# Kernel tuning notes

Hardware: AMD Instinct MI355X
Metric: run time of the kernel (lower is better)

The kernel has to match this reference:

```python
import jax, jax.numpy as jnp
import numpy as np

B, T, C, H = 4, 2048, 1024, 16
D = C // H  # head_size = 64


def _layernorm(x, g, b, eps=1e-5):
    mu = jnp.mean(x, axis=-1, keepdims=True)
    var = jnp.var(x, axis=-1, keepdims=True)
    return (x - mu) * jax.lax.rsqrt(var + eps) * g + b


def setup_inputs() -> dict:
    key = jax.random.key(0)
    ks = jax.random.split(key, 12)
    s = 0.02
    return {
        "x": jax.random.normal(ks[0], (B, T, C), dtype=jnp.float32),
        "Wq": jax.random.normal(ks[1], (C, C), dtype=jnp.float32) * s,
        "Wk": jax.random.normal(ks[2], (C, C), dtype=jnp.float32) * s,
        "Wv": jax.random.normal(ks[3], (C, C), dtype=jnp.float32) * s,
        "Wo": jax.random.normal(ks[4], (C, C), dtype=jnp.float32) * s,
        "bo": jnp.zeros((C,), dtype=jnp.float32),
        "ln1_g": jnp.ones((C,), dtype=jnp.float32),
        "ln1_b": jnp.zeros((C,), dtype=jnp.float32),
        "ln2_g": jnp.ones((C,), dtype=jnp.float32),
        "ln2_b": jnp.zeros((C,), dtype=jnp.float32),
        "W1": jax.random.normal(ks[5], (C, 4 * C), dtype=jnp.float32) * s,
        "b1": jnp.zeros((4 * C,), dtype=jnp.float32),
        "W2": jax.random.normal(ks[6], (4 * C, C), dtype=jnp.float32) * s,
        "b2": jnp.zeros((C,), dtype=jnp.float32),
    }


def reference(x, Wq, Wk, Wv, Wo, bo, ln1_g, ln1_b, ln2_g, ln2_b, W1, b1, W2, b2):
    # --- self-attention branch (pre-LN) ---
    h = _layernorm(x, ln1_g, ln1_b)
    q = (h @ Wq).reshape(B, T, H, D)
    k = (h @ Wk).reshape(B, T, H, D)
    v = (h @ Wv).reshape(B, T, H, D)
    scores = jnp.einsum("bqhd,bkhd->bhqk", q, k) * (D ** -0.5)
    causal = jnp.tril(jnp.ones((T, T), dtype=bool))
    scores = jnp.where(causal, scores, -jnp.inf)
    attn = jax.nn.softmax(scores, axis=-1)  # dropout=0 in eval
    out = jnp.einsum("bhqk,bkhd->bqhd", attn, v).reshape(B, T, C)
    x = x + (out @ Wo + bo)
    # --- feed-forward branch (pre-LN) ---
    h2 = _layernorm(x, ln2_g, ln2_b)
    ff = jax.nn.relu(h2 @ W1 + b1) @ W2 + b2
    return x + ff
```

## Files before the change

### kernel.cpp

```cpp
#include <hip/hip_runtime.h>
#include <hip/hip_bf16.h>
#include <math.h>

#define Bsz 4
#define Tsz 2048
#define Csz 1024
#define Hsz 16
#define Dsz 64
#define Msz (Bsz * Tsz)

typedef __attribute__((ext_vector_type(8))) __bf16 bf16x8;
typedef __attribute__((ext_vector_type(2))) __bf16 bf16x2;
typedef __attribute__((ext_vector_type(4))) float f32x4;

#define GLOBAL_AS __attribute__((address_space(1)))
#define LDS_AS    __attribute__((address_space(3)))


__device__ __forceinline__ float block_sum256(float v, float* sh) {
#pragma unroll
    for (int o = 32; o > 0; o >>= 1) v += __shfl_down(v, o, 64);
    int lane = threadIdx.x & 63, w = threadIdx.x >> 6;
    __syncthreads();
    if (lane == 0) sh[w] = v;
    __syncthreads();
    return sh[0] + sh[1] + sh[2] + sh[3];
}


__global__ __launch_bounds__(256) void layernorm_bf16(const float* __restrict__ x,
                                                      const float* __restrict__ g,
                                                      const float* __restrict__ b,
                                                      __bf16* __restrict__ out) {
    __shared__ float sh[4];
    const int row = blockIdx.x;
    const float* xr = x + (size_t)row * Csz;
    float v[4];
    float s = 0.f, ss = 0.f;
#pragma unroll
    for (int i = 0; i < 4; i++) {
        v[i] = xr[threadIdx.x + i * 256];
        s += v[i];
        ss += v[i] * v[i];
    }
    float tot = block_sum256(s, sh);
    float mean = tot * (1.0f / Csz);
    float tot2 = block_sum256(ss, sh);
    float var = tot2 * (1.0f / Csz) - mean * mean;
    float inv = rsqrtf(var + 1e-5f);
    __bf16* orow = out + (size_t)row * Csz;
#pragma unroll
    for (int i = 0; i < 4; i++) {
        int c = threadIdx.x + i * 256;
        orow[c] = (__bf16)((v[i] - mean) * inv * g[c] + b[c]);
    }
}


__global__ __launch_bounds__(256) void transpose_bf16(const float* __restrict__ W,
                                                      __bf16* __restrict__ Wt,
                                                      int K, int N) {
    __shared__ float t[32][33];
    const int k0 = blockIdx.y * 32, n0 = blockIdx.x * 32;
    const int c = threadIdx.x & 31, r8 = threadIdx.x >> 5;
#pragma unroll
    for (int it = 0; it < 4; it++) {
        int r = r8 + it * 8;
        t[r][c] = W[(size_t)(k0 + r) * N + n0 + c];
    }
    __syncthreads();
#pragma unroll
    for (int it = 0; it < 4; it++) {
        int r = r8 + it * 8;
        Wt[(size_t)(n0 + r) * K + k0 + c] = (__bf16)t[c][r];
    }
}


__global__ __launch_bounds__(256) void gemm_bf16(const __bf16* __restrict__ A,
                                                 const __bf16* __restrict__ Bt,
                                                 float* __restrict__ Cf,
                                                 __bf16* __restrict__ Cb,
                                                 int M, int N, int K,
                                                 const float* __restrict__ bias,
                                                 const float* __restrict__ resid,
                                                 int do_relu) {
    __shared__ __bf16 As[128 * 32];
    __shared__ __bf16 Bs[128 * 32];

    const int tid = threadIdx.x;
    const int lane = tid & 63;
    const int w = tid >> 6;
    const int rowBase = blockIdx.y * 128;
    const int colBase = blockIdx.x * 128;
    const int wr = (w & 1) * 64;
    const int wc = (w >> 1) * 64;

    const int m16 = lane & 15;
    const int kg = lane >> 4;

    f32x4 acc[4][4] = {};

    const int ldRow = lane >> 2;
    const int ldCol = (lane & 3) * 8;

    for (int k0 = 0; k0 < K; k0 += 32) {
        __syncthreads();
#pragma unroll
        for (int j = 0; j < 2; j++) {
            int rA = w * 32 + j * 16 + ldRow;
            const __bf16* ga = A + (size_t)(rowBase + rA) * K + k0 + ldCol;
            __builtin_amdgcn_global_load_lds((const GLOBAL_AS unsigned int*)ga,
                                             (LDS_AS unsigned int*)(As + rA * 32),
                                             16, 0, 0);
            int rB = w * 32 + j * 16 + ldRow;
            const __bf16* gb = Bt + (size_t)(colBase + rB) * K + k0 + ldCol;
            __builtin_amdgcn_global_load_lds((const GLOBAL_AS unsigned int*)gb,
                                             (LDS_AS unsigned int*)(Bs + rB * 32),
                                             16, 0, 0);
        }
        __syncthreads();

        bf16x8 af[4], bfv[4];
#pragma unroll
        for (int i = 0; i < 4; i++)
            af[i] = *(const bf16x8*)(As + (wr + i * 16 + m16) * 32 + kg * 8);
#pragma unroll
        for (int j = 0; j < 4; j++)
            bfv[j] = *(const bf16x8*)(Bs + (wc + j * 16 + m16) * 32 + kg * 8);
#pragma unroll
        for (int i = 0; i < 4; i++)
#pragma unroll
            for (int j = 0; j < 4; j++)
                acc[i][j] = __builtin_amdgcn_mfma_f32_16x16x32_bf16(af[i], bfv[j], acc[i][j], 0, 0, 0);
    }

    const int cn = lane & 15;
    const int rq = (lane >> 4) * 4;
    float bj[4];
#pragma unroll
    for (int j = 0; j < 4; j++)
        bj[j] = bias ? bias[colBase + wc + j * 16 + cn] : 0.f;

#pragma unroll
    for (int i = 0; i < 4; i++) {
#pragma unroll
        for (int r = 0; r < 4; r++) {
            int m = rowBase + wr + i * 16 + rq + r;
            size_t rowOff = (size_t)m * N;
#pragma unroll
            for (int j = 0; j < 4; j++) {
                int n = colBase + wc + j * 16 + cn;
                float v = acc[i][j][r] + bj[j];
                if (do_relu) v = fmaxf(v, 0.f);
                if (resid) v += resid[rowOff + n];
                if (Cf) Cf[rowOff + n] = v;
                if (Cb) Cb[rowOff + n] = (__bf16)v;
            }
        }
    }
}


__global__ __launch_bounds__(256, 4) void attn_mfma(const __bf16* __restrict__ QKV,
                                                    __bf16* __restrict__ O) {
    __shared__ __bf16 Ks[64 * 64];
    __shared__ __bf16 Vt[64 * 72];
    __shared__ __bf16 Ps[128 * 72];

    const int tid = threadIdx.x;
    const int lane = tid & 63;
    const int w = tid >> 6;
    const int bh = blockIdx.x;
    const int b = bh >> 4, h = bh & 15;
    const int qt = (int)gridDim.y - 1 - (int)blockIdx.y;
    const int qbase = qt * 128;
    const int ld3C = 3 * Csz;

    const __bf16* Qg = QKV + (size_t)(b * Tsz) * ld3C + h * Dsz;
    const __bf16* Kg = Qg + Csz;
    const __bf16* Vg = Qg + 2 * Csz;

    const int m16 = lane & 15;
    const int kg = lane >> 4;
    const int rq = kg * 4;
    const int wrow = w * 32;
    const int swz = m16 & 7;

    bf16x8 aq[2][2];
#pragma unroll
    for (int i = 0; i < 2; i++)
#pragma unroll
        for (int s = 0; s < 2; s++)
            aq[i][s] = *(const bf16x8*)(Qg + (size_t)(qbase + wrow + i * 16 + m16) * ld3C + (s * 4 + kg) * 8);

    const int sr = lane >> 3;
    const int sc = lane & 7;
    const int gcs = sc ^ sr;

    const int kp = (lane & 31) * 2;
    const int dg = w * 2 + (lane >> 5);

    f32x4 Oacc[2][4];
    float l_part[2][4];
#pragma unroll
    for (int i = 0; i < 2; i++)
#pragma unroll
        for (int j = 0; j < 4; j++) Oacc[i][j] = (f32x4){0.f, 0.f, 0.f, 0.f};
#pragma unroll
    for (int i = 0; i < 2; i++)
#pragma unroll
        for (int r = 0; r < 4; r++) l_part[i][r] = 0.f;

    const float CEXP = 0.18033688f;

    const int nkt = 2 * qt + 2;
    for (int kt = 0; kt < nkt; kt++) {
        const int kbase = kt * 64;
        __syncthreads();

#pragma unroll
        for (int it = 0; it < 2; it++) {
            int lr = w * 16 + it * 8 + sr;
            const __bf16* src = Kg + (size_t)(kbase + lr) * ld3C + gcs * 8;
            __builtin_amdgcn_global_load_lds((const GLOBAL_AS unsigned int*)src,
                                             (LDS_AS unsigned int*)(Ks + (w * 16 + it * 8) * 64),
                                             16, 0, 0);
        }
        bf16x8 v0 = *(const bf16x8*)(Vg + (size_t)(kbase + kp) * ld3C + dg * 8);
        bf16x8 v1 = *(const bf16x8*)(Vg + (size_t)(kbase + kp + 1) * ld3C + dg * 8);
        __syncthreads();

        f32x4 S[2][4];
#pragma unroll
        for (int i = 0; i < 2; i++)
#pragma unroll
            for (int j = 0; j < 4; j++) S[i][j] = (f32x4){0.f, 0.f, 0.f, 0.f};
#pragma unroll
        for (int s = 0; s < 2; s++) {
            bf16x8 bk[4];
#pragma unroll
            for (int j = 0; j < 4; j++)
                bk[j] = *(const bf16x8*)(Ks + (j * 16 + m16) * 64 + (((s * 4 + kg) ^ swz) * 8));
#pragma unroll
            for (int i = 0; i < 2; i++)
#pragma unroll
                for (int j = 0; j < 4; j++)
                    S[i][j] = __builtin_amdgcn_mfma_f32_16x16x32_bf16(aq[i][s], bk[j], S[i][j], 0, 0, 0);
        }

        const bool domask = (kt >= 2 * qt);
#pragma unroll
        for (int i = 0; i < 2; i++) {
#pragma unroll
            for (int j = 0; j < 4; j++) {
#pragma unroll
                for (int r = 0; r < 4; r++) {
                    float arg = S[i][j][r] * CEXP;
                    if (domask && (kbase + j * 16 + m16 > qbase + wrow + i * 16 + rq + r))
                        arg = -INFINITY;
                    float e = exp2f(arg);
                    S[i][j][r] = e;
                    l_part[i][r] += e;
                }
            }
        }

#pragma unroll
        for (int i = 0; i < 2; i++)
#pragma unroll
            for (int j = 0; j < 4; j++)
#pragma unroll
                for (int r = 0; r < 4; r++)
                    Ps[(wrow + i * 16 + rq + r) * 72 + j * 16 + m16] = (__bf16)S[i][j][r];
#pragma unroll
        for (int e = 0; e < 8; e++) {
            bf16x2 pr;
            pr[0] = v0[e];
            pr[1] = v1[e];
            *(bf16x2*)(Vt + (dg * 8 + e) * 72 + kp) = pr;
        }
        __syncthreads();

#pragma unroll
        for (int s = 0; s < 2; s++) {
            bf16x8 ap[2], bv[4];
#pragma unroll
            for (int i = 0; i < 2; i++)
                ap[i] = *(const bf16x8*)(Ps + (wrow + i * 16 + m16) * 72 + s * 32 + kg * 8);
#pragma unroll
            for (int j = 0; j < 4; j++)
                bv[j] = *(const bf16x8*)(Vt + (j * 16 + m16) * 72 + s * 32 + kg * 8);
#pragma unroll
            for (int i = 0; i < 2; i++)
#pragma unroll
                for (int j = 0; j < 4; j++)
                    Oacc[i][j] = __builtin_amdgcn_mfma_f32_16x16x32_bf16(ap[i], bv[j], Oacc[i][j], 0, 0, 0);
        }
    }

#pragma unroll
    for (int i = 0; i < 2; i++) {
#pragma unroll
        for (int r = 0; r < 4; r++) {
            float l = l_part[i][r];
#pragma unroll
            for (int msk = 1; msk < 16; msk <<= 1) l += __shfl_xor(l, msk, 64);
            const float inv = 1.0f / l;
            const int qrow = qbase + wrow + i * 16 + rq + r;
            __bf16* orow = O + (size_t)(b * Tsz + qrow) * Csz + h * Dsz;
#pragma unroll
            for (int j = 0; j < 4; j++)
                orow[j * 16 + m16] = (__bf16)(Oacc[i][j][r] * inv);
        }
    }
}


extern "C" void kernel_launch(void* const* d_in, const int* in_sizes, int n_in,
                              void* d_out, int out_size, void* d_ws, size_t ws_size,
                              hipStream_t stream) {
    const float* x     = (const float*)d_in[0];
    const float* Wq    = (const float*)d_in[1];
    const float* Wk    = (const float*)d_in[2];
    const float* Wv    = (const float*)d_in[3];
    const float* Wo    = (const float*)d_in[4];
    const float* bo    = (const float*)d_in[5];
    const float* ln1_g = (const float*)d_in[6];
    const float* ln1_b = (const float*)d_in[7];
    const float* ln2_g = (const float*)d_in[8];
    const float* ln2_b = (const float*)d_in[9];
    const float* W1    = (const float*)d_in[10];
    const float* b1    = (const float*)d_in[11];
    const float* W2    = (const float*)d_in[12];
    const float* b2    = (const float*)d_in[13];
    float* out = (float*)d_out;

    const size_t MB = 1u << 20;
    char* w = (char*)d_ws;
    __bf16* h    = (__bf16*)(w + 0);
    __bf16* Wqkv = (__bf16*)(w + 16 * MB);
    __bf16* Wot  = (__bf16*)(w + 22 * MB);
    __bf16* W1t  = (__bf16*)(w + 24 * MB);
    __bf16* W2t  = (__bf16*)(w + 32 * MB);
    __bf16* QKVb = (__bf16*)(w + 40 * MB);
    __bf16* ff1  = (__bf16*)(w + 40 * MB);
    __bf16* AO   = (__bf16*)(w + 104 * MB);

    transpose_bf16<<<dim3(Csz / 32, Csz / 32), 256, 0, stream>>>(Wq, Wqkv, Csz, Csz);
    transpose_bf16<<<dim3(Csz / 32, Csz / 32), 256, 0, stream>>>(Wk, Wqkv + 1024 * 1024, Csz, Csz);
    transpose_bf16<<<dim3(Csz / 32, Csz / 32), 256, 0, stream>>>(Wv, Wqkv + 2048 * 1024, Csz, Csz);
    transpose_bf16<<<dim3(Csz / 32, Csz / 32), 256, 0, stream>>>(Wo, Wot, Csz, Csz);
    transpose_bf16<<<dim3(4 * Csz / 32, Csz / 32), 256, 0, stream>>>(W1, W1t, Csz, 4 * Csz);
    transpose_bf16<<<dim3(Csz / 32, 4 * Csz / 32), 256, 0, stream>>>(W2, W2t, 4 * Csz, Csz);

    layernorm_bf16<<<Msz, 256, 0, stream>>>(x, ln1_g, ln1_b, h);
    gemm_bf16<<<dim3(3 * Csz / 128, Msz / 128), 256, 0, stream>>>(h, Wqkv, nullptr, QKVb, Msz, 3 * Csz, Csz, nullptr, nullptr, 0);
    attn_mfma<<<dim3(Bsz * Hsz, Tsz / 128), 256, 0, stream>>>(QKVb, AO);
    gemm_bf16<<<dim3(Csz / 128, Msz / 128), 256, 0, stream>>>(AO, Wot, out, nullptr, Msz, Csz, Csz, bo, x, 0);

    layernorm_bf16<<<Msz, 256, 0, stream>>>(out, ln2_g, ln2_b, h);
    gemm_bf16<<<dim3(4 * Csz / 128, Msz / 128), 256, 0, stream>>>(h, W1t, nullptr, ff1, Msz, 4 * Csz, Csz, b1, nullptr, 1);
    gemm_bf16<<<dim3(Csz / 128, Msz / 128), 256, 0, stream>>>(ff1, W2t, out, nullptr, Msz, Csz, 4 * Csz, b2, out, 0);
}
```

Baseline: 599.4 us.

## Use swizzled BK=64 GEMM tiles, split-K FFN down-proj, batch weight transposes

GEMM K-tile doubles to 64 with an XOR-swizzled LDS layout to halve barrier count per K and reduce bank conflicts. The FFN second GEMM is split along K into two halves via blockIdx.z, with a separate kernel summing the partial and bias, to raise block count. The four square weight transposes are merged into one launch. Split-K adds an extra fp32 read/write pass over the output.

```diff
diff --git a/kernel.cpp b/kernel.cpp
--- a/kernel.cpp
+++ b/kernel.cpp
@@ -76,17 +76,44 @@
     }
 }
 
+__global__ __launch_bounds__(256) void transpose4_bf16(const float* __restrict__ Wa,
+                                                       const float* __restrict__ Wb,
+                                                       const float* __restrict__ Wc,
+                                                       const float* __restrict__ Wd,
+                                                       __bf16* __restrict__ Ta,
+                                                       __bf16* __restrict__ Tb,
+                                                       __bf16* __restrict__ Tc,
+                                                       __bf16* __restrict__ Td) {
+    __shared__ float t[32][33];
+    const float* W = (blockIdx.z == 0) ? Wa : (blockIdx.z == 1) ? Wb : (blockIdx.z == 2) ? Wc : Wd;
+    __bf16* Wt = (blockIdx.z == 0) ? Ta : (blockIdx.z == 1) ? Tb : (blockIdx.z == 2) ? Tc : Td;
+    const int k0 = blockIdx.y * 32, n0 = blockIdx.x * 32;
+    const int c = threadIdx.x & 31, r8 = threadIdx.x >> 5;
+#pragma unroll
+    for (int it = 0; it < 4; it++) {
+        int r = r8 + it * 8;
+        t[r][c] = W[(size_t)(k0 + r) * Csz + n0 + c];
+    }
+    __syncthreads();
+#pragma unroll
+    for (int it = 0; it < 4; it++) {
+        int r = r8 + it * 8;
+        Wt[(size_t)(n0 + r) * Csz + k0 + c] = (__bf16)t[c][r];
+    }
+}
+
 
 __global__ __launch_bounds__(256) void gemm_bf16(const __bf16* __restrict__ A,
                                                  const __bf16* __restrict__ Bt,
                                                  float* __restrict__ Cf,
+                                                 float* __restrict__ Cf2,
                                                  __bf16* __restrict__ Cb,
-                                                 int M, int N, int K,
+                                                 int M, int N, int K, int ld,
                                                  const float* __restrict__ bias,
                                                  const float* __restrict__ resid,
                                                  int do_relu) {
-    __shared__ __bf16 As[128 * 32];
-    __shared__ __bf16 Bs[128 * 32];
+    __shared__ __bf16 As[128 * 64];
+    __shared__ __bf16 Bs[128 * 64];
 
     const int tid = threadIdx.x;
     const int lane = tid & 63;
@@ -96,43 +123,55 @@
     const int wr = (w & 1) * 64;
     const int wc = (w >> 1) * 64;
 
+    const __bf16* Ak = A + (size_t)blockIdx.z * K;
+    const __bf16* Bk = Bt + (size_t)blockIdx.z * K;
+    float* Cfu = Cf;
+    const float* residu = resid;
+    const float* biasu = bias;
+    if (blockIdx.z == 1) { Cfu = Cf2; residu = nullptr; biasu = nullptr; }
+
     const int m16 = lane & 15;
     const int kg = lane >> 4;
+    const int swz = m16 & 7;
+
+    const int sr = lane >> 3;
+    const int sc = lane & 7;
+    const int gcs = sc ^ sr;
 
     f32x4 acc[4][4] = {};
 
-    const int ldRow = lane >> 2;
-    const int ldCol = (lane & 3) * 8;
-
-    for (int k0 = 0; k0 < K; k0 += 32) {
+    for (int k0 = 0; k0 < K; k0 += 64) {
         __syncthreads();
 #pragma unroll
-        for (int j = 0; j < 2; j++) {
-            int rA = w * 32 + j * 16 + ldRow;
-            const __bf16* ga = A + (size_t)(rowBase + rA) * K + k0 + ldCol;
+        for (int it = 0; it < 4; it++) {
+            int lr = w * 32 + it * 8;
+            const __bf16* ga = Ak + (size_t)(rowBase + lr + sr) * ld + k0 + gcs * 8;
             __builtin_amdgcn_global_load_lds((const GLOBAL_AS unsigned int*)ga,
-                                             (LDS_AS unsigned int*)(As + rA * 32),
+                                             (LDS_AS unsigned int*)(As + lr * 64),
                                              16, 0, 0);
-            int rB = w * 32 + j * 16 + ldRow;
-            const __bf16* gb = Bt + (size_t)(colBase + rB) * K + k0 + ldCol;
+            const __bf16* gb = Bk + (size_t)(colBase + lr + sr) * ld + k0 + gcs * 8;
             __builtin_amdgcn_global_load_lds((const GLOBAL_AS unsigned int*)gb,
-                                             (LDS_AS unsigned int*)(Bs + rB * 32),
+                                             (LDS_AS unsigned int*)(Bs + lr * 64),
                                              16, 0, 0);
         }
         __syncthreads();
 
-        bf16x8 af[4], bfv[4];
-#pragma unroll
-        for (int i = 0; i < 4; i++)
-            af[i] = *(const bf16x8*)(As + (wr + i * 16 + m16) * 32 + kg * 8);
-#pragma unroll
-        for (int j = 0; j < 4; j++)
-            bfv[j] = *(const bf16x8*)(Bs + (wc + j * 16 + m16) * 32 + kg * 8);
-#pragma unroll
-        for (int i = 0; i < 4; i++)
+#pragma unroll
+        for (int s = 0; s < 2; s++) {
+            const int slot = ((s * 4 + kg) ^ swz) * 8;
+            bf16x8 af[4], bfv[4];
+#pragma unroll
+            for (int i = 0; i < 4; i++)
+                af[i] = *(const bf16x8*)(As + (wr + i * 16 + m16) * 64 + slot);
 #pragma unroll
             for (int j = 0; j < 4; j++)
-                acc[i][j] = __builtin_amdgcn_mfma_f32_16x16x32_bf16(af[i], bfv[j], acc[i][j], 0, 0, 0);
+                bfv[j] = *(const bf16x8*)(Bs + (wc + j * 16 + m16) * 64 + slot);
+#pragma unroll
+            for (int i = 0; i < 4; i++)
+#pragma unroll
+                for (int j = 0; j < 4; j++)
+                    acc[i][j] = __builtin_amdgcn_mfma_f32_16x16x32_bf16(af[i], bfv[j], acc[i][j], 0, 0, 0);
+        }
     }
 
     const int cn = lane & 15;
@@ -140,7 +179,7 @@
     float bj[4];
 #pragma unroll
     for (int j = 0; j < 4; j++)
-        bj[j] = bias ? bias[colBase + wc + j * 16 + cn] : 0.f;
+        bj[j] = biasu ? biasu[colBase + wc + j * 16 + cn] : 0.f;
 
 #pragma unroll
     for (int i = 0; i < 4; i++) {
@@ -153,12 +192,27 @@
                 int n = colBase + wc + j * 16 + cn;
                 float v = acc[i][j][r] + bj[j];
                 if (do_relu) v = fmaxf(v, 0.f);
-                if (resid) v += resid[rowOff + n];
-                if (Cf) Cf[rowOff + n] = v;
-                if (Cb) Cb[rowOff + n] = (__bf16)v;
+                if (residu) v += residu[rowOff + n];
+                if (Cfu) Cfu[rowOff + n] = v;
+                if (Cb && blockIdx.z == 0) Cb[rowOff + n] = (__bf16)v;
             }
         }
     }
+}
+
+
+__global__ __launch_bounds__(256) void add_partial(float* __restrict__ out,
+                                                   const float* __restrict__ p,
+                                                   const float* __restrict__ b2) {
+    size_t i = ((size_t)blockIdx.x * 256 + threadIdx.x) * 4;
+    float4 o = *(float4*)(out + i);
+    const float4 a = *(const float4*)(p + i);
+    const float4 bb = *(const float4*)(b2 + (i & (Csz - 1)));
+    o.x += a.x + bb.x;
+    o.y += a.y + bb.y;
+    o.z += a.z + bb.z;
+    o.w += a.w + bb.w;
+    *(float4*)(out + i) = o;
 }
 
 
@@ -344,22 +398,26 @@
     __bf16* W1t  = (__bf16*)(w + 24 * MB);
     __bf16* W2t  = (__bf16*)(w + 32 * MB);
     __bf16* QKVb = (__bf16*)(w + 40 * MB);
+    __bf16* AO   = (__bf16*)(w + 88 * MB);
     __bf16* ff1  = (__bf16*)(w + 40 * MB);
-    __bf16* AO   = (__bf16*)(w + 104 * MB);
-
-    transpose_bf16<<<dim3(Csz / 32, Csz / 32), 256, 0, stream>>>(Wq, Wqkv, Csz, Csz);
-    transpose_bf16<<<dim3(Csz / 32, Csz / 32), 256, 0, stream>>>(Wk, Wqkv + 1024 * 1024, Csz, Csz);
-    transpose_bf16<<<dim3(Csz / 32, Csz / 32), 256, 0, stream>>>(Wv, Wqkv + 2048 * 1024, Csz, Csz);
-    transpose_bf16<<<dim3(Csz / 32, Csz / 32), 256, 0, stream>>>(Wo, Wot, Csz, Csz);
+    float*  p1   = (float*)(w + 0);
+
+    transpose4_bf16<<<dim3(32, 32, 4), 256, 0, stream>>>(Wq, Wk, Wv, Wo,
+                                                         Wqkv, Wqkv + 1024 * 1024, Wqkv + 2048 * 1024, Wot);
     transpose_bf16<<<dim3(4 * Csz / 32, Csz / 32), 256, 0, stream>>>(W1, W1t, Csz, 4 * Csz);
     transpose_bf16<<<dim3(Csz / 32, 4 * Csz / 32), 256, 0, stream>>>(W2, W2t, 4 * Csz, Csz);
 
     layernorm_bf16<<<Msz, 256, 0, stream>>>(x, ln1_g, ln1_b, h);
-    gemm_bf16<<<dim3(3 * Csz / 128, Msz / 128), 256, 0, stream>>>(h, Wqkv, nullptr, QKVb, Msz, 3 * Csz, Csz, nullptr, nullptr, 0);
+    gemm_bf16<<<dim3(3 * Csz / 128, Msz / 128), 256, 0, stream>>>(
+        h, Wqkv, nullptr, nullptr, QKVb, Msz, 3 * Csz, Csz, Csz, nullptr, nullptr, 0);
     attn_mfma<<<dim3(Bsz * Hsz, Tsz / 128), 256, 0, stream>>>(QKVb, AO);
-    gemm_bf16<<<dim3(Csz / 128, Msz / 128), 256, 0, stream>>>(AO, Wot, out, nullptr, Msz, Csz, Csz, bo, x, 0);
+    gemm_bf16<<<dim3(Csz / 128, Msz / 128), 256, 0, stream>>>(
+        AO, Wot, out, nullptr, nullptr, Msz, Csz, Csz, Csz, bo, x, 0);
 
     layernorm_bf16<<<Msz, 256, 0, stream>>>(out, ln2_g, ln2_b, h);
-    gemm_bf16<<<dim3(4 * Csz / 128, Msz / 128), 256, 0, stream>>>(h, W1t, nullptr, ff1, Msz, 4 * Csz, Csz, b1, nullptr, 1);
-    gemm_bf16<<<dim3(Csz / 128, Msz / 128), 256, 0, stream>>>(ff1, W2t, out, nullptr, Msz, Csz, 4 * Csz, b2, out, 0);
-}
+    gemm_bf16<<<dim3(4 * Csz / 128, Msz / 128), 256, 0, stream>>>(
+        h, W1t, nullptr, nullptr, ff1, Msz, 4 * Csz, Csz, Csz, b1, nullptr, 1);
+    gemm_bf16<<<dim3(Csz / 128, Msz / 128, 2), 256, 0, stream>>>(
+        ff1, W2t, out, p1, nullptr, Msz, Csz, 2 * Csz, 4 * Csz, nullptr, out, 0);
+    add_partial<<<Msz * Csz / 1024, 256, 0, stream>>>(out, p1, b2);
+}
```

New measurement: 562.3 us. 6.2% less time.
